# Performance work log

Measured on AMD Instinct MI355X. Metric: run time of the kernel, lower is better.

## Reference

```python
import jax, jax.numpy as jnp
import numpy as np

TOL = 1e-6          # Rattle.__init__ tol
NEWTON_ITERS = 4    # con is affine in lmd, so Newton converges at iter 1; extras are guarded no-ops


def setup_inputs() -> dict:
    key = jax.random.key(0)
    k1, k2, k3 = jax.random.split(key, 3)
    B, C, N = 64, 64, 4096  # replicas, constraints, atoms
    mom = jax.random.normal(k1, (B, N, 3), jnp.float32)                  # momenta
    mas = jax.random.uniform(k2, (B, N), jnp.float32, 0.5, 2.0)          # positive masses
    dtm = jnp.full((B,), 1e-3, jnp.float32)                              # timestep
    jac_prv = jax.random.normal(k3, (B, C, N, 3), jnp.float32)           # constraint Jacobian
    return {"mom": mom, "mas": mas, "dtm": dtm, "jac_prv": jac_prv}


def _rattle(mom, mas, dtm, jac_prv):
    # A = jac_prv / mas  (mass-weighted Jacobian), shape [B,C,N,3]
    A = jac_prv / mas[:, None, :, None]
    # Newton Jacobian d(con)/d(lmd): constant because con is affine in lmd.
    # J[b,i,j] = -dtm * sum_{n,d} jac_prv[b,i,n,d]/mas[b,n] * jac_prv[b,j,n,d]
    J = -dtm[:, None, None] * jnp.einsum('bind,bjnd->bij', A, jac_prv)

    def con_fn(lmd):
        # tmp = mom - (jac_prv * lmd).sum(C) * dtm ; con = (A * tmp).sum(N,3)
        tmp = mom - dtm[:, None, None] * jnp.einsum('bc,bcnd->bnd', lmd, jac_prv)
        return jnp.einsum('bcnd,bnd->bc', A, tmp)

    lmd0 = jnp.zeros(jac_prv.shape[:2], mom.dtype)  # [B,C]

    def step(lmd, _):
        con = con_fn(lmd)
        # torch.solve(con[:,:,None], jac): solve J @ dlt = con, batched over B
        dlt = jnp.linalg.solve(J, con[..., None])[..., 0]
        converged = jnp.max(jnp.abs(con)) < TOL
        lmd = jnp.where(converged, lmd, lmd - dlt)
        return lmd, None

    lmd, _ = jax.lax.scan(step, lmd0, None, length=NEWTON_ITERS)

    # out momentum: mom + frc*dtm with frc = -(lmd * jac_prv).sum(C)
    mom_out = mom - dtm[:, None, None] * jnp.einsum('bc,bcnd->bnd', lmd, jac_prv)
    return mom_out, lmd


def reference(mom, mas, dtm, jac_prv):
    return _rattle(mom, mas, dtm, jac_prv)
```

## Files before the change

kernel.cpp:

```cpp
#include <hip/hip_runtime.h>


namespace {
constexpr int Bb = 64;
constexpr int Cc = 64;
constexpr int Kk = 12288;
constexpr int QB = 8;
constexpr int KCHUNK = Kk / QB;
constexpr size_t J8_BYTES = (size_t)Bb * Cc * Kk;
constexpr size_t GPART_FLOATS = (size_t)Bb * QB * 4096;
constexpr size_t C0_FLOATS = (size_t)Bb * QB * 64;
constexpr size_t WS_NEED = J8_BYTES + (GPART_FLOATS + C0_FLOATS) * 4;
}

typedef __attribute__((ext_vector_type(8))) __bf16 bf16x8;
typedef __attribute__((ext_vector_type(16))) float f32x16;
typedef __attribute__((ext_vector_type(2))) float f32x2;

template <bool WRITE8>
__global__ __launch_bounds__(256) void k1_gram(const float* __restrict__ jac,
                                               const float* __restrict__ mas,
                                               const float* __restrict__ mom,
                                               float* __restrict__ Gpart,
                                               float* __restrict__ c0part,
                                               unsigned char* __restrict__ jac8) {
    __shared__ __align__(16) __bf16 AhL[64 * 64];
    __shared__ __align__(16) __bf16 BhL[64 * 64];
    __shared__ __align__(16) float wLds[KCHUNK];
    __shared__ float c0red[4][64];

    const int b   = blockIdx.x >> 3;
    const int qb  = blockIdx.x & 7;
    const int tid = threadIdx.x;
    const int kbeg = qb * KCHUNK;

    for (int kk = tid; kk < KCHUNK; kk += 256)
        wLds[kk] = 1.0f / mas[b * 4096 + (kbeg + kk) / 3];

    const int cS = tid >> 2, gS = tid & 3;
    const float* jrow = jac + (size_t)(b * 64 + cS) * Kk;
    const float* momB = mom + (size_t)b * Kk;
    unsigned char* j8row = jac8 + (size_t)(b * 64 + cS) * Kk;
    const int swzS = (cS & 7) << 3;

    const int w = tid >> 6, lane = tid & 63;
    const int i0 = (w & 1) << 5, j0 = (w >> 1) << 5;
    const int r = lane & 31, kg = lane >> 5;
    const int arow = i0 + r, brow = j0 + r;
    const int abase = arow * 64, aswz = (arow & 7) << 3;
    const int bbase = brow * 64, bswz = (brow & 7) << 3;

    f32x16 acc;
#pragma unroll
    for (int z = 0; z < 16; ++z) acc[z] = 0.0f;
    float c0acc = 0.0f;

    __syncthreads();

    for (int t = 0; t < KCHUNK / 64; ++t) {
        const int k0 = kbeg + t * 64;
        const float4* jp = (const float4*)(jrow + k0 + gS * 16);
        const float4* wp = (const float4*)(wLds + (k0 - kbeg) + gS * 16);
        const float4* mp = (const float4*)(momB + k0 + gS * 16);

        bf16x8 ah[2], bh[2];
        int pk[4];
#pragma unroll
        for (int v = 0; v < 4; ++v) {
            float4 x = jp[v];
            float4 wv = wp[v];
            float4 m = mp[v];
            float y0 = x.x * wv.x, y1 = x.y * wv.y, y2 = x.z * wv.z, y3 = x.w * wv.w;
            c0acc += y0 * m.x + y1 * m.y + y2 * m.z + y3 * m.w;
            const int h = v >> 1, e0 = (v & 1) * 4;
            ah[h][e0 + 0] = (__bf16)y0; ah[h][e0 + 1] = (__bf16)y1;
            ah[h][e0 + 2] = (__bf16)y2; ah[h][e0 + 3] = (__bf16)y3;
            bh[h][e0 + 0] = (__bf16)x.x; bh[h][e0 + 1] = (__bf16)x.y;
            bh[h][e0 + 2] = (__bf16)x.z; bh[h][e0 + 3] = (__bf16)x.w;
            if (WRITE8) {
                int lo = __builtin_amdgcn_cvt_pk_fp8_f32(x.x, x.y, 0, false);
                pk[v]  = __builtin_amdgcn_cvt_pk_fp8_f32(x.z, x.w, lo, true);
            }
        }
        if (WRITE8) {
            uint4 u = {(unsigned)pk[0], (unsigned)pk[1], (unsigned)pk[2], (unsigned)pk[3]};
            *(uint4*)(j8row + k0 + gS * 16) = u;
        }
#pragma unroll
        for (int h = 0; h < 2; ++h) {
            const int off = cS * 64 + ((gS * 16 + h * 8) ^ swzS);
            *(bf16x8*)&AhL[off] = ah[h];
            *(bf16x8*)&BhL[off] = bh[h];
        }
        __syncthreads();

#pragma unroll
        for (int ks = 0; ks < 4; ++ks) {
            const int kc = ks * 16 + kg * 8;
            bf16x8 a  = *(const bf16x8*)&AhL[abase + (kc ^ aswz)];
            bf16x8 bb = *(const bf16x8*)&BhL[bbase + (kc ^ bswz)];
            acc = __builtin_amdgcn_mfma_f32_32x32x16_bf16(a, bb, acc, 0, 0, 0);
        }
        __syncthreads();
    }

    float* Gp = Gpart + (size_t)(b * QB + qb) * 4096;
#pragma unroll
    for (int reg = 0; reg < 16; ++reg) {
        const int row = (reg & 3) + 8 * (reg >> 2) + 4 * kg;
        Gp[(i0 + row) * 64 + (j0 + r)] = acc[reg];
    }

    c0red[gS][cS] = c0acc;
    __syncthreads();
    if (tid < 64)
        c0part[(b * QB + qb) * 64 + tid] =
            c0red[0][tid] + c0red[1][tid] + c0red[2][tid] + c0red[3][tid];
}

__global__ __launch_bounds__(256) void k2_solve(const float* __restrict__ Gpart,
                                                const float* __restrict__ c0part,
                                                const float* __restrict__ dtm,
                                                float* __restrict__ lmd_out) {
    __shared__ __align__(16) float G[64][68];
    __shared__ float red[2][4][64];
    __shared__ float zw[4][64];

    const int b = blockIdx.x;
    const int t = threadIdx.x;
    const int i = t & 63, q = t >> 6;

    for (int e4 = t * 4; e4 < 4096; e4 += 1024) {
        float4 s = {0.0f, 0.0f, 0.0f, 0.0f};
#pragma unroll
        for (int qq = 0; qq < QB; ++qq) {
            float4 v = *(const float4*)&Gpart[(size_t)(b * QB + qq) * 4096 + e4];
            s.x += v.x; s.y += v.y; s.z += v.z; s.w += v.w;
        }
        *(float4*)&G[e4 >> 6][e4 & 63] = s;
    }
    float c0 = 0.0f;
#pragma unroll
    for (int qq = 0; qq < QB; ++qq) c0 += c0part[(b * QB + qq) * 64 + i];
    __syncthreads();

    const float invD = 1.0f / G[i][i];
    float z = c0 * invD;
    zw[q][i] = z;

    for (int it = 0; it < 10; ++it) {
        float s = 0.0f;
        const float* gr = &G[i][q * 16];
        const float* zr = &zw[q][q * 16];
#pragma unroll
        for (int g = 0; g < 4; ++g) {
            float4 g4 = *(const float4*)&gr[4 * g];
            float4 z4 = *(const float4*)&zr[4 * g];
            s += g4.x * z4.x + g4.y * z4.y + g4.z * z4.z + g4.w * z4.w;
        }
        const int p = it & 1;
        red[p][q][i] = s;
        __syncthreads();
        const float rres = c0 - (red[p][0][i] + red[p][1][i] + red[p][2][i] + red[p][3][i]);
        z += rres * invD;
        zw[q][i] = z;
    }

    if (t < 64) lmd_out[b * 64 + t] = z * (1.0f / dtm[b]);
}

__global__ __launch_bounds__(256) void k3_momout_fp8(const unsigned char* __restrict__ jac8,
                                                     const float* __restrict__ mom,
                                                     const float* __restrict__ dtm,
                                                     const float* __restrict__ lmd,
                                                     float* __restrict__ mom_out) {
    __shared__ float lLds[64];
    const int b   = blockIdx.y;
    const int blk = blockIdx.x;
    const int t   = threadIdx.x;
    if (t < 64) lLds[t] = lmd[b * 64 + t];
    __syncthreads();

    const int kbase = blk * 2048 + t * 8;
    const unsigned char* jp = jac8 + (size_t)b * Cc * Kk + kbase;

    float acc[8];
#pragma unroll
    for (int z = 0; z < 8; ++z) acc[z] = 0.0f;

#pragma unroll 4
    for (int c = 0; c < 64; ++c) {
        uint2 u = *(const uint2*)(jp + (size_t)c * Kk);
        const float lc = lLds[c];
        f32x2 d;
        d = __builtin_amdgcn_cvt_pk_f32_fp8(u.x, false); acc[0] += lc * d[0]; acc[1] += lc * d[1];
        d = __builtin_amdgcn_cvt_pk_f32_fp8(u.x, true);  acc[2] += lc * d[0]; acc[3] += lc * d[1];
        d = __builtin_amdgcn_cvt_pk_f32_fp8(u.y, false); acc[4] += lc * d[0]; acc[5] += lc * d[1];
        d = __builtin_amdgcn_cvt_pk_f32_fp8(u.y, true);  acc[6] += lc * d[0]; acc[7] += lc * d[1];
    }
    const float dt = dtm[b];
    const float* mb = mom + (size_t)b * Kk + kbase;
    float4 m0 = *(const float4*)mb;
    float4 m1 = *(const float4*)(mb + 4);
    float4 o0, o1;
    o0.x = m0.x - dt * acc[0]; o0.y = m0.y - dt * acc[1];
    o0.z = m0.z - dt * acc[2]; o0.w = m0.w - dt * acc[3];
    o1.x = m1.x - dt * acc[4]; o1.y = m1.y - dt * acc[5];
    o1.z = m1.z - dt * acc[6]; o1.w = m1.w - dt * acc[7];
    float* ob = mom_out + (size_t)b * Kk + kbase;
    *(float4*)ob = o0;
    *(float4*)(ob + 4) = o1;
}

__global__ __launch_bounds__(256) void k3_momout(const float* __restrict__ jac,
                                                 const float* __restrict__ mom,
                                                 const float* __restrict__ dtm,
                                                 const float* __restrict__ lmd,
                                                 float* __restrict__ mom_out) {
    __shared__ float lLds[64];
    const int b   = blockIdx.y;
    const int blk = blockIdx.x;
    const int t   = threadIdx.x;
    if (t < 64) lLds[t] = lmd[b * 64 + t];
    __syncthreads();

    const size_t kbase = (size_t)blk * 1024 + (size_t)t * 4;
    const float* jp = jac + (size_t)b * Cc * Kk + kbase;

    float4 acc = {0.0f, 0.0f, 0.0f, 0.0f};
#pragma unroll 4
    for (int c = 0; c < 64; ++c) {
        float4 jv = *(const float4*)(jp + (size_t)c * Kk);
        float lc = lLds[c];
        acc.x += lc * jv.x;
        acc.y += lc * jv.y;
        acc.z += lc * jv.z;
        acc.w += lc * jv.w;
    }
    const float dt = dtm[b];
    float4 m4 = *(const float4*)(mom + (size_t)b * Kk + kbase);
    float4 o;
    o.x = m4.x - dt * acc.x;
    o.y = m4.y - dt * acc.y;
    o.z = m4.z - dt * acc.z;
    o.w = m4.w - dt * acc.w;
    *(float4*)(mom_out + (size_t)b * Kk + kbase) = o;
}

extern "C" void kernel_launch(void* const* d_in, const int* in_sizes, int n_in,
                              void* d_out, int out_size, void* d_ws, size_t ws_size,
                              hipStream_t stream) {
    const float* mom = (const float*)d_in[0];
    const float* mas = (const float*)d_in[1];
    const float* dtm = (const float*)d_in[2];
    const float* jac = (const float*)d_in[3];

    float* out = (float*)d_out;
    float* lmd = out + (size_t)Bb * Kk;

    const bool use_fp8 = ws_size >= WS_NEED;

    unsigned char* jac8 = (unsigned char*)d_ws;
    float* Gpart;
    float* c0part;
    if (use_fp8) {
        Gpart = (float*)(jac8 + J8_BYTES);
        c0part = Gpart + GPART_FLOATS;
    } else {
        Gpart = (float*)d_ws;
        c0part = Gpart + GPART_FLOATS;
    }

    if (use_fp8) {
        k1_gram<true><<<Bb * QB, 256, 0, stream>>>(jac, mas, mom, Gpart, c0part, jac8);
        k2_solve<<<Bb, 256, 0, stream>>>(Gpart, c0part, dtm, lmd);
        k3_momout_fp8<<<dim3(6, 64), 256, 0, stream>>>(jac8, mom, dtm, lmd, out);
    } else {
        k1_gram<false><<<Bb * QB, 256, 0, stream>>>(jac, mas, mom, Gpart, c0part, nullptr);
        k2_solve<<<Bb, 256, 0, stream>>>(Gpart, c0part, dtm, lmd);
        k3_momout<<<dim3(12, 64), 256, 0, stream>>>(jac, mom, dtm, lmd, out);
    }
}
```

Measured before the change: 66.95 us.

## Split Gram K-chunks finer, widen solve block, use nontemporal loads/stores

Doubles the K split in the Gram kernel from 8 to 16 chunks, giving 1024 blocks and a launch-bounds occupancy hint. The solve kernel now uses 1024 threads with a 16-way partial dot reduction and drops the Jacobi-style iterations from 10 to 8. Streaming loads of jac and mom and the output stores become nontemporal, and the fp8 momentum loop is unrolled further. The finer split doubles partial-Gram traffic into the solve kernel, and fewer iterations may loosen accuracy.

After: 105.8 us. +58.1%, slower.

```diff
diff --git a/kernel.cpp b/kernel.cpp
--- a/kernel.cpp
+++ b/kernel.cpp
@@ -5,8 +5,9 @@
 constexpr int Bb = 64;
 constexpr int Cc = 64;
 constexpr int Kk = 12288;
-constexpr int QB = 8;
+constexpr int QB = 16;
 constexpr int KCHUNK = Kk / QB;
+constexpr int NT = KCHUNK / 64;
 constexpr size_t J8_BYTES = (size_t)Bb * Cc * Kk;
 constexpr size_t GPART_FLOATS = (size_t)Bb * QB * 4096;
 constexpr size_t C0_FLOATS = (size_t)Bb * QB * 64;
@@ -15,22 +16,24 @@
 
 typedef __attribute__((ext_vector_type(8))) __bf16 bf16x8;
 typedef __attribute__((ext_vector_type(16))) float f32x16;
+typedef __attribute__((ext_vector_type(4))) float f32x4;
 typedef __attribute__((ext_vector_type(2))) float f32x2;
+typedef __attribute__((ext_vector_type(4))) unsigned int u32x4;
 
 template <bool WRITE8>
-__global__ __launch_bounds__(256) void k1_gram(const float* __restrict__ jac,
-                                               const float* __restrict__ mas,
-                                               const float* __restrict__ mom,
-                                               float* __restrict__ Gpart,
-                                               float* __restrict__ c0part,
-                                               unsigned char* __restrict__ jac8) {
+__global__ __launch_bounds__(256, 4) void k1_gram(const float* __restrict__ jac,
+                                                  const float* __restrict__ mas,
+                                                  const float* __restrict__ mom,
+                                                  float* __restrict__ Gpart,
+                                                  float* __restrict__ c0part,
+                                                  unsigned char* __restrict__ jac8) {
     __shared__ __align__(16) __bf16 AhL[64 * 64];
     __shared__ __align__(16) __bf16 BhL[64 * 64];
     __shared__ __align__(16) float wLds[KCHUNK];
     __shared__ float c0red[4][64];
 
-    const int b   = blockIdx.x >> 3;
-    const int qb  = blockIdx.x & 7;
+    const int b   = blockIdx.x >> 4;
+    const int qb  = blockIdx.x & 15;
     const int tid = threadIdx.x;
     const int kbeg = qb * KCHUNK;
 
@@ -57,19 +60,19 @@
 
     __syncthreads();
 
-    for (int t = 0; t < KCHUNK / 64; ++t) {
+    for (int t = 0; t < NT; ++t) {
         const int k0 = kbeg + t * 64;
-        const float4* jp = (const float4*)(jrow + k0 + gS * 16);
-        const float4* wp = (const float4*)(wLds + (k0 - kbeg) + gS * 16);
-        const float4* mp = (const float4*)(momB + k0 + gS * 16);
+        const f32x4* jp = (const f32x4*)(jrow + k0 + gS * 16);
+        const f32x4* wp = (const f32x4*)(wLds + (k0 - kbeg) + gS * 16);
+        const f32x4* mp = (const f32x4*)(momB + k0 + gS * 16);
 
         bf16x8 ah[2], bh[2];
         int pk[4];
 #pragma unroll
         for (int v = 0; v < 4; ++v) {
-            float4 x = jp[v];
-            float4 wv = wp[v];
-            float4 m = mp[v];
+            f32x4 x = __builtin_nontemporal_load(&jp[v]);
+            f32x4 wv = wp[v];
+            f32x4 m = __builtin_nontemporal_load(&mp[v]);
             float y0 = x.x * wv.x, y1 = x.y * wv.y, y2 = x.z * wv.z, y3 = x.w * wv.w;
             c0acc += y0 * m.x + y1 * m.y + y2 * m.z + y3 * m.w;
             const int h = v >> 1, e0 = (v & 1) * 4;
@@ -83,8 +86,8 @@
             }
         }
         if (WRITE8) {
-            uint4 u = {(unsigned)pk[0], (unsigned)pk[1], (unsigned)pk[2], (unsigned)pk[3]};
-            *(uint4*)(j8row + k0 + gS * 16) = u;
+            u32x4 u = {(unsigned)pk[0], (unsigned)pk[1], (unsigned)pk[2], (unsigned)pk[3]};
+            *(u32x4*)(j8row + k0 + gS * 16) = u;
         }
 #pragma unroll
         for (int h = 0; h < 2; ++h) {
@@ -118,26 +121,26 @@
             c0red[0][tid] + c0red[1][tid] + c0red[2][tid] + c0red[3][tid];
 }
 
-__global__ __launch_bounds__(256) void k2_solve(const float* __restrict__ Gpart,
-                                                const float* __restrict__ c0part,
-                                                const float* __restrict__ dtm,
-                                                float* __restrict__ lmd_out) {
+__global__ __launch_bounds__(1024) void k2_solve(const float* __restrict__ Gpart,
+                                                 const float* __restrict__ c0part,
+                                                 const float* __restrict__ dtm,
+                                                 float* __restrict__ lmd_out) {
     __shared__ __align__(16) float G[64][68];
-    __shared__ float red[2][4][64];
-    __shared__ float zw[4][64];
+    __shared__ float red[2][16][64];
+    __shared__ float zw[16][64];
 
     const int b = blockIdx.x;
     const int t = threadIdx.x;
     const int i = t & 63, q = t >> 6;
 
-    for (int e4 = t * 4; e4 < 4096; e4 += 1024) {
+    {
         float4 s = {0.0f, 0.0f, 0.0f, 0.0f};
 #pragma unroll
         for (int qq = 0; qq < QB; ++qq) {
-            float4 v = *(const float4*)&Gpart[(size_t)(b * QB + qq) * 4096 + e4];
+            float4 v = *(const float4*)&Gpart[(size_t)(b * QB + qq) * 4096 + t * 4];
             s.x += v.x; s.y += v.y; s.z += v.z; s.w += v.w;
         }
-        *(float4*)&G[e4 >> 6][e4 & 63] = s;
+        *(float4*)&G[t >> 4][(t & 15) * 4] = s;
     }
     float c0 = 0.0f;
 #pragma unroll
@@ -148,20 +151,16 @@
     float z = c0 * invD;
     zw[q][i] = z;
 
-    for (int it = 0; it < 10; ++it) {
-        float s = 0.0f;
-        const float* gr = &G[i][q * 16];
-        const float* zr = &zw[q][q * 16];
-#pragma unroll
-        for (int g = 0; g < 4; ++g) {
-            float4 g4 = *(const float4*)&gr[4 * g];
-            float4 z4 = *(const float4*)&zr[4 * g];
-            s += g4.x * z4.x + g4.y * z4.y + g4.z * z4.z + g4.w * z4.w;
-        }
+    for (int it = 0; it < 8; ++it) {
+        float4 g4 = *(const float4*)&G[i][q * 4];
+        float4 z4 = *(const float4*)&zw[q][q * 4];
+        float s = g4.x * z4.x + g4.y * z4.y + g4.z * z4.z + g4.w * z4.w;
         const int p = it & 1;
         red[p][q][i] = s;
         __syncthreads();
-        const float rres = c0 - (red[p][0][i] + red[p][1][i] + red[p][2][i] + red[p][3][i]);
+        float rres = c0;
+#pragma unroll
+        for (int qq = 0; qq < 16; ++qq) rres -= red[p][qq][i];
         z += rres * invD;
         zw[q][i] = z;
     }
@@ -188,7 +187,7 @@
 #pragma unroll
     for (int z = 0; z < 8; ++z) acc[z] = 0.0f;
 
-#pragma unroll 4
+#pragma unroll 8
     for (int c = 0; c < 64; ++c) {
         uint2 u = *(const uint2*)(jp + (size_t)c * Kk);
         const float lc = lLds[c];
@@ -202,14 +201,14 @@
     const float* mb = mom + (size_t)b * Kk + kbase;
     float4 m0 = *(const float4*)mb;
     float4 m1 = *(const float4*)(mb + 4);
-    float4 o0, o1;
+    f32x4 o0, o1;
     o0.x = m0.x - dt * acc[0]; o0.y = m0.y - dt * acc[1];
     o0.z = m0.z - dt * acc[2]; o0.w = m0.w - dt * acc[3];
     o1.x = m1.x - dt * acc[4]; o1.y = m1.y - dt * acc[5];
     o1.z = m1.z - dt * acc[6]; o1.w = m1.w - dt * acc[7];
     float* ob = mom_out + (size_t)b * Kk + kbase;
-    *(float4*)ob = o0;
-    *(float4*)(ob + 4) = o1;
+    __builtin_nontemporal_store(o0, (f32x4*)ob);
+    __builtin_nontemporal_store(o1, (f32x4*)(ob + 4));
 }
 
 __global__ __launch_bounds__(256) void k3_momout(const float* __restrict__ jac,
@@ -273,11 +272,11 @@
 
     if (use_fp8) {
         k1_gram<true><<<Bb * QB, 256, 0, stream>>>(jac, mas, mom, Gpart, c0part, jac8);
-        k2_solve<<<Bb, 256, 0, stream>>>(Gpart, c0part, dtm, lmd);
+        k2_solve<<<Bb, 1024, 0, stream>>>(Gpart, c0part, dtm, lmd);
         k3_momout_fp8<<<dim3(6, 64), 256, 0, stream>>>(jac8, mom, dtm, lmd, out);
     } else {
         k1_gram<false><<<Bb * QB, 256, 0, stream>>>(jac, mas, mom, Gpart, c0part, nullptr);
-        k2_solve<<<Bb, 256, 0, stream>>>(Gpart, c0part, dtm, lmd);
+        k2_solve<<<Bb, 1024, 0, stream>>>(Gpart, c0part, dtm, lmd);
         k3_momout<<<dim3(12, 64), 256, 0, stream>>>(jac, mom, dtm, lmd, out);
     }
 }
```

## Double Gram kernel block size with split-K across waves and fewer Jacobi iterations

Applied to the files above, without the earlier changes.

The Gram kernel now runs 512 threads per block. Each thread loads half as many Jacobian elements per tile. Waves are split into two K-halves that each do two MFMA steps, and their accumulators are combined through shared memory at the end. This is meant to raise memory-level parallelism and occupancy in the bandwidth-bound first pass. The solve kernel also drops from 10 to 8 Jacobi refinement iterations, which trades a little convergence margin for less latency.

After: 65.10 us. 1.03x faster.

```diff
diff --git a/kernel.cpp b/kernel.cpp
--- a/kernel.cpp
+++ b/kernel.cpp
@@ -7,6 +7,7 @@
 constexpr int Kk = 12288;
 constexpr int QB = 8;
 constexpr int KCHUNK = Kk / QB;
+constexpr int NT = KCHUNK / 64;
 constexpr size_t J8_BYTES = (size_t)Bb * Cc * Kk;
 constexpr size_t GPART_FLOATS = (size_t)Bb * QB * 4096;
 constexpr size_t C0_FLOATS = (size_t)Bb * QB * 64;
@@ -18,7 +19,7 @@
 typedef __attribute__((ext_vector_type(2))) float f32x2;
 
 template <bool WRITE8>
-__global__ __launch_bounds__(256) void k1_gram(const float* __restrict__ jac,
+__global__ __launch_bounds__(512) void k1_gram(const float* __restrict__ jac,
                                                const float* __restrict__ mas,
                                                const float* __restrict__ mom,
                                                float* __restrict__ Gpart,
@@ -27,24 +28,26 @@
     __shared__ __align__(16) __bf16 AhL[64 * 64];
     __shared__ __align__(16) __bf16 BhL[64 * 64];
     __shared__ __align__(16) float wLds[KCHUNK];
-    __shared__ float c0red[4][64];
+    __shared__ float c0red[8][64];
+    __shared__ float accred[4][64][17];
 
     const int b   = blockIdx.x >> 3;
     const int qb  = blockIdx.x & 7;
     const int tid = threadIdx.x;
     const int kbeg = qb * KCHUNK;
 
-    for (int kk = tid; kk < KCHUNK; kk += 256)
+    for (int kk = tid; kk < KCHUNK; kk += 512)
         wLds[kk] = 1.0f / mas[b * 4096 + (kbeg + kk) / 3];
 
-    const int cS = tid >> 2, gS = tid & 3;
+    const int cS = tid >> 3, gS = tid & 7;
     const float* jrow = jac + (size_t)(b * 64 + cS) * Kk;
     const float* momB = mom + (size_t)b * Kk;
     unsigned char* j8row = jac8 + (size_t)(b * 64 + cS) * Kk;
     const int swzS = (cS & 7) << 3;
 
     const int w = tid >> 6, lane = tid & 63;
-    const int i0 = (w & 1) << 5, j0 = (w >> 1) << 5;
+    const int qd = w & 3, khalf = w >> 2;
+    const int i0 = (qd & 1) << 5, j0 = (qd >> 1) << 5;
     const int r = lane & 31, kg = lane >> 5;
     const int arow = i0 + r, brow = j0 + r;
     const int abase = arow * 64, aswz = (arow & 7) << 3;
@@ -57,45 +60,45 @@
 
     __syncthreads();
 
-    for (int t = 0; t < KCHUNK / 64; ++t) {
+    for (int t = 0; t < NT; ++t) {
         const int k0 = kbeg + t * 64;
-        const float4* jp = (const float4*)(jrow + k0 + gS * 16);
-        const float4* wp = (const float4*)(wLds + (k0 - kbeg) + gS * 16);
-        const float4* mp = (const float4*)(momB + k0 + gS * 16);
-
-        bf16x8 ah[2], bh[2];
-        int pk[4];
-#pragma unroll
-        for (int v = 0; v < 4; ++v) {
+        const float4* jp = (const float4*)(jrow + k0 + gS * 8);
+        const float4* wp = (const float4*)(wLds + (k0 - kbeg) + gS * 8);
+        const float4* mp = (const float4*)(momB + k0 + gS * 8);
+
+        bf16x8 ah, bh;
+        int pk[2];
+#pragma unroll
+        for (int v = 0; v < 2; ++v) {
             float4 x = jp[v];
             float4 wv = wp[v];
             float4 m = mp[v];
             float y0 = x.x * wv.x, y1 = x.y * wv.y, y2 = x.z * wv.z, y3 = x.w * wv.w;
             c0acc += y0 * m.x + y1 * m.y + y2 * m.z + y3 * m.w;
-            const int h = v >> 1, e0 = (v & 1) * 4;
-            ah[h][e0 + 0] = (__bf16)y0; ah[h][e0 + 1] = (__bf16)y1;
-            ah[h][e0 + 2] = (__bf16)y2; ah[h][e0 + 3] = (__bf16)y3;
-            bh[h][e0 + 0] = (__bf16)x.x; bh[h][e0 + 1] = (__bf16)x.y;
-            bh[h][e0 + 2] = (__bf16)x.z; bh[h][e0 + 3] = (__bf16)x.w;
+            const int e0 = v * 4;
+            ah[e0 + 0] = (__bf16)y0; ah[e0 + 1] = (__bf16)y1;
+            ah[e0 + 2] = (__bf16)y2; ah[e0 + 3] = (__bf16)y3;
+            bh[e0 + 0] = (__bf16)x.x; bh[e0 + 1] = (__bf16)x.y;
+            bh[e0 + 2] = (__bf16)x.z; bh[e0 + 3] = (__bf16)x.w;
             if (WRITE8) {
                 int lo = __builtin_amdgcn_cvt_pk_fp8_f32(x.x, x.y, 0, false);
                 pk[v]  = __builtin_amdgcn_cvt_pk_fp8_f32(x.z, x.w, lo, true);
             }
         }
         if (WRITE8) {
-            uint4 u = {(unsigned)pk[0], (unsigned)pk[1], (unsigned)pk[2], (unsigned)pk[3]};
-            *(uint4*)(j8row + k0 + gS * 16) = u;
-        }
-#pragma unroll
-        for (int h = 0; h < 2; ++h) {
-            const int off = cS * 64 + ((gS * 16 + h * 8) ^ swzS);
-            *(bf16x8*)&AhL[off] = ah[h];
-            *(bf16x8*)&BhL[off] = bh[h];
+            uint2 u = {(unsigned)pk[0], (unsigned)pk[1]};
+            *(uint2*)(j8row + k0 + gS * 8) = u;
+        }
+        {
+            const int off = cS * 64 + ((gS * 8) ^ swzS);
+            *(bf16x8*)&AhL[off] = ah;
+            *(bf16x8*)&BhL[off] = bh;
         }
         __syncthreads();
 
 #pragma unroll
-        for (int ks = 0; ks < 4; ++ks) {
+        for (int s = 0; s < 2; ++s) {
+            const int ks = khalf * 2 + s;
             const int kc = ks * 16 + kg * 8;
             bf16x8 a  = *(const bf16x8*)&AhL[abase + (kc ^ aswz)];
             bf16x8 bb = *(const bf16x8*)&BhL[bbase + (kc ^ bswz)];
@@ -104,18 +107,27 @@
         __syncthreads();
     }
 
-    float* Gp = Gpart + (size_t)(b * QB + qb) * 4096;
-#pragma unroll
-    for (int reg = 0; reg < 16; ++reg) {
-        const int row = (reg & 3) + 8 * (reg >> 2) + 4 * kg;
-        Gp[(i0 + row) * 64 + (j0 + r)] = acc[reg];
-    }
-
+    if (khalf == 1) {
+#pragma unroll
+        for (int z = 0; z < 16; ++z) accred[qd][lane][z] = acc[z];
+    }
     c0red[gS][cS] = c0acc;
     __syncthreads();
-    if (tid < 64)
-        c0part[(b * QB + qb) * 64 + tid] =
-            c0red[0][tid] + c0red[1][tid] + c0red[2][tid] + c0red[3][tid];
+
+    if (khalf == 0) {
+        float* Gp = Gpart + (size_t)(b * QB + qb) * 4096;
+#pragma unroll
+        for (int reg = 0; reg < 16; ++reg) {
+            const int row = (reg & 3) + 8 * (reg >> 2) + 4 * kg;
+            Gp[(i0 + row) * 64 + (j0 + r)] = acc[reg] + accred[qd][lane][reg];
+        }
+    }
+    if (tid < 64) {
+        float s = 0.0f;
+#pragma unroll
+        for (int g = 0; g < 8; ++g) s += c0red[g][tid];
+        c0part[(b * QB + qb) * 64 + tid] = s;
+    }
 }
 
 __global__ __launch_bounds__(256) void k2_solve(const float* __restrict__ Gpart,
@@ -148,7 +160,7 @@
     float z = c0 * invD;
     zw[q][i] = z;
 
-    for (int it = 0; it < 10; ++it) {
+    for (int it = 0; it < 8; ++it) {
         float s = 0.0f;
         const float* gr = &G[i][q * 16];
         const float* zr = &zw[q][q * 16];
@@ -272,11 +284,11 @@
     }
 
     if (use_fp8) {
-        k1_gram<true><<<Bb * QB, 256, 0, stream>>>(jac, mas, mom, Gpart, c0part, jac8);
+        k1_gram<true><<<Bb * QB, 512, 0, stream>>>(jac, mas, mom, Gpart, c0part, jac8);
         k2_solve<<<Bb, 256, 0, stream>>>(Gpart, c0part, dtm, lmd);
         k3_momout_fp8<<<dim3(6, 64), 256, 0, stream>>>(jac8, mom, dtm, lmd, out);
     } else {
-        k1_gram<false><<<Bb * QB, 256, 0, stream>>>(jac, mas, mom, Gpart, c0part, nullptr);
+        k1_gram<false><<<Bb * QB, 512, 0, stream>>>(jac, mas, mom, Gpart, c0part, nullptr);
         k2_solve<<<Bb, 256, 0, stream>>>(Gpart, c0part, dtm, lmd);
         k3_momout<<<dim3(12, 64), 256, 0, stream>>>(jac, mom, dtm, lmd, out);
     }
```
